# Optimization experiments

Measured on AMD Instinct MI355X. Metric: run time of the kernel, lower is better.

## Reference

```python
import jax, jax.numpy as jnp
import numpy as np

EPS = 1e-5  # rms_norm_eps

def rmsnorm(x, w, eps=EPS):
    xf = x.astype(jnp.float32)
    n = xf * jax.lax.rsqrt(jnp.mean(xf * xf, axis=-1, keepdims=True) + eps)
    return n.astype(x.dtype) * w

def setup_inputs() -> dict:
    key = jax.random.key(0)
    ks = jax.random.split(key, 8)
    B, S, E = 2, 2048, 2048
    H, M, D = 16, 2048, 128  # heads, memory slots, head_dim; H*D == E
    return {
        "query": jax.random.normal(ks[0], (B, S, E), jnp.float32),
        "storedpatterns": jax.random.normal(ks[1], (H, M, D), jnp.float32) * 0.02,
        "wq": jax.random.normal(ks[2], (H * D, E), jnp.float32) * (1.0 / np.sqrt(E)),
        "wk": jax.random.normal(ks[3], (D, D), jnp.float32) * (1.0 / np.sqrt(D)),
        "wv": jax.random.normal(ks[4], (D, D), jnp.float32) * (1.0 / np.sqrt(D)),
        "beta": jnp.ones((1, H, 1, 1), jnp.float32),
        "norm_q_w": jnp.ones((E,), jnp.float32),
        "norm_r_w": jnp.ones((H * D,), jnp.float32),
    }

def reference(query, storedpatterns, wq, wk, wv, beta, norm_q_w, norm_r_w):
    B, S, E = query.shape
    H, M, D = storedpatterns.shape
    # RMSNorm query, project to multi-head queries [B,H,S,D]
    qn = rmsnorm(query, norm_q_w)
    q = jnp.einsum('bse,fe->bsf', qn, wq).reshape(B, S, H, D).transpose(0, 2, 1, 3)
    # per-head K/V projections of stored memory patterns [H,M,D]
    k = jnp.einsum('hmd,ed->hme', storedpatterns, wk)
    v = jnp.einsum('hmd,ed->hme', storedpatterns, wv)
    # beta-scaled attention over memory slots
    scores = jnp.einsum('bhsd,hmd->bhsm', q, k) * beta / jnp.sqrt(jnp.float32(D))
    attn = jax.nn.softmax(scores, axis=-1)
    retrieved = jnp.einsum('bhsm,hmd->bhsd', attn, v)  # [B,H,S,D]
    retrieved = retrieved.transpose(0, 2, 1, 3).reshape(B, S, H * D)
    retrieved = rmsnorm(retrieved, norm_r_w)
    # combine_method='add' (pattern_dim == emb_dim, no dim projection)
    return query + retrieved
```

## Files before the change

kernel.cpp:

```cpp
#include <hip/hip_runtime.h>
#include <hip/hip_bf16.h>
#include <stdint.h>

typedef __attribute__((ext_vector_type(8))) short bf16x8;
typedef __attribute__((ext_vector_type(4))) float f32x4;
typedef __attribute__((ext_vector_type(8))) unsigned short u16x8;
typedef __attribute__((ext_vector_type(4))) unsigned short u16x4;
typedef __attribute__((ext_vector_type(2))) unsigned long long ull2;
typedef __attribute__((ext_vector_type(8))) int i32x8;

#define B_ 2
#define S_ 2048
#define E_ 2048
#define H_ 16
#define M_ 2048
#define D_ 128

#define MFMA16(a, b, c) __builtin_amdgcn_mfma_f32_16x16x32_bf16(a, b, c, 0, 0, 0)
#define MFMA8(a, b, c) __builtin_amdgcn_mfma_f32_16x16x32_fp8_fp8(a, b, c, 0, 0, 0)
#define MFMAS(a, b, c) __builtin_amdgcn_mfma_scale_f32_16x16x128_f8f6f4( \
    a, b, c, 0, 0, 0, 127, 0, 127)

union U32x8 { ull2 u2[2]; long long q[4]; i32x8 v; };

__device__ inline unsigned short f2bf(float f) {
  union { float f; unsigned u; } v; v.f = f;
  unsigned r = v.u + 0x7FFFu + ((v.u >> 16) & 1u);
  return (unsigned short)(r >> 16);
}
__device__ inline float bf2f(unsigned short h) {
  union { unsigned u; float f; } v; v.u = ((unsigned)h) << 16;
  return v.f;
}

__device__ inline unsigned char f2e8(float f) {
  return (unsigned char)(__builtin_amdgcn_cvt_pk_fp8_f32(f, f, 0, false) & 0xFF);
}
__device__ inline uint32_t pk4e8(float a, float b, float c, float d) {
  uint32_t w = 0;
  w = (uint32_t)__builtin_amdgcn_cvt_pk_fp8_f32(a, b, (int)w, false);
  w = (uint32_t)__builtin_amdgcn_cvt_pk_fp8_f32(c, d, (int)w, true);
  return w;
}

__device__ inline float exp2a(float x) {
  float r;
  asm("v_exp_f32 %0, %1" : "=v"(r) : "v"(x));
  return r;
}

__device__ inline void gload_lds16(const void* g, void* l) {
  __builtin_amdgcn_global_load_lds(
      (__attribute__((address_space(1))) void*)g,
      (__attribute__((address_space(3))) void*)l, 16, 0, 0);
}

__device__ inline bf16x8 pack8(float4 f0, float4 f1) {
  bf16x8 o;
  o[0] = (short)f2bf(f0.x); o[1] = (short)f2bf(f0.y);
  o[2] = (short)f2bf(f0.z); o[3] = (short)f2bf(f0.w);
  o[4] = (short)f2bf(f1.x); o[5] = (short)f2bf(f1.y);
  o[6] = (short)f2bf(f1.z); o[7] = (short)f2bf(f1.w);
  return o;
}

__device__ inline float block_sum(float v) {
  __shared__ float red[4];
  #pragma unroll
  for (int o = 32; o > 0; o >>= 1) v += __shfl_xor(v, o);
  int tid = threadIdx.x;
  if ((tid & 63) == 0) red[tid >> 6] = v;
  __syncthreads();
  return red[0] + red[1] + red[2] + red[3];
}

__device__ inline int pi_pos(int c) {
  return (c & ~127) | (((c >> 3) & 3) * 32) | (((c >> 5) & 3) * 8) | (c & 7);
}

#define PREP_PROJ 512
#define PREP_CONV 2048
#define PREP_NORM 4096
__global__ __launch_bounds__(256, 2) void prep_kernel(
    const float* __restrict__ query, const float* __restrict__ sp,
    const float* __restrict__ wq, const float* __restrict__ wk,
    const float* __restrict__ wv, const float* __restrict__ nqw,
    unsigned char* __restrict__ wqb, unsigned char* __restrict__ qn,
    unsigned char* __restrict__ kout, unsigned char* __restrict__ vtout)
{
  const int bid = blockIdx.x;
  const int tid = threadIdx.x;

  if (bid < PREP_PROJ) {
    const int idx = bid;
    const int m0 = (idx & 31) * 64;
    const int h = idx >> 5;
    const int wave = tid >> 6, lane = tid & 63;
    const int r = lane & 15, g = lane >> 4;
    const int wm = (wave >> 1) * 32, wn = (wave & 1) * 64;
    const float* spb = sp + ((size_t)h * M_ + m0) * D_;
    f32x4 acck[2][4] = {};
    f32x4 accv[2][4] = {};
    #pragma unroll
    for (int kc = 0; kc < 4; ++kc) {
      bf16x8 a[2], bk[4], bv[4];
      #pragma unroll
      for (int m = 0; m < 2; ++m) {
        const float* p = spb + (size_t)(wm + m * 16 + r) * D_ + kc * 32 + g * 8;
        a[m] = pack8(*(const float4*)p, *(const float4*)(p + 4));
      }
      #pragma unroll
      for (int n = 0; n < 4; ++n) {
        const float* pk = wk + (size_t)(wn + n * 16 + r) * D_ + kc * 32 + g * 8;
        bk[n] = pack8(*(const float4*)pk, *(const float4*)(pk + 4));
        const float* pv = wv + (size_t)(wn + n * 16 + r) * D_ + kc * 32 + g * 8;
        bv[n] = pack8(*(const float4*)pv, *(const float4*)(pv + 4));
      }
      #pragma unroll
      for (int m = 0; m < 2; ++m)
        #pragma unroll
        for (int n = 0; n < 4; ++n) {
          acck[m][n] = MFMA16(a[m], bk[n], acck[m][n]);
          accv[m][n] = MFMA16(a[m], bv[n], accv[m][n]);
        }
    }
    #pragma unroll
    for (int m = 0; m < 2; ++m)
      #pragma unroll
      for (int n = 0; n < 4; ++n)
        #pragma unroll
        for (int i = 0; i < 4; ++i) {
          int d = wn + n * 16 + r;
          kout[((size_t)h * M_ + m0 + wm + m * 16 + g * 4 + i) * D_ + pi_pos(d)]
              = f2e8(acck[m][n][i] * 32.0f);
          int mc = m0 + wm + m * 16 + g * 4 + i;
          int mp = (mc & ~127) | (pi_pos(mc & 127));
          vtout[((size_t)h * D_ + wn + n * 16 + r) * M_ + mp]
              = f2e8(accv[m][n][i] * 32.0f);
        }
  } else if (bid < PREP_PROJ + PREP_CONV) {
    int i = (bid - PREP_PROJ) * 256 + tid;
    const float* p = wq + (size_t)i * 8;
    float4 a = *(const float4*)p, b = *(const float4*)(p + 4);
    uint2 pk;
    pk.x = pk4e8(a.x, a.y, a.z, a.w);
    pk.y = pk4e8(b.x, b.y, b.z, b.w);
    size_t flat = (size_t)i * 8;
    int c = (int)(flat & (E_ - 1));
    *(uint2*)(wqb + (flat - c) + pi_pos(c)) = pk;
  } else {
    const int row = bid - (PREP_PROJ + PREP_CONV);
    const float* xr = query + (size_t)row * E_;
    float4 v0 = ((const float4*)xr)[tid * 2];
    float4 v1 = ((const float4*)xr)[tid * 2 + 1];
    float ss = v0.x*v0.x + v0.y*v0.y + v0.z*v0.z + v0.w*v0.w
             + v1.x*v1.x + v1.y*v1.y + v1.z*v1.z + v1.w*v1.w;
    float tot = block_sum(ss);
    float sc = rsqrtf(tot * (1.0f / E_) + 1e-5f);
    float vals[8] = {v0.x, v0.y, v0.z, v0.w, v1.x, v1.y, v1.z, v1.w};
    const float* wr = nqw + tid * 8;
    float f[8];
    #pragma unroll
    for (int j = 0; j < 8; ++j) f[j] = vals[j] * sc * wr[j];
    uint2 pk;
    pk.x = pk4e8(f[0], f[1], f[2], f[3]);
    pk.y = pk4e8(f[4], f[5], f[6], f[7]);
    *(uint2*)(qn + (size_t)row * E_ + pi_pos(tid * 8)) = pk;
  }
}

__global__ __launch_bounds__(256) void gemm_qproj(
    const unsigned char* __restrict__ A, const unsigned char* __restrict__ B,
    unsigned char* __restrict__ C, int M, int N, int K)
{
  __shared__ __align__(16) unsigned char As[128 * 128];
  __shared__ __align__(16) unsigned char Bs[128 * 128];
  const int nwg = gridDim.x;
  const int cpx = nwg >> 3;
  const int swz = (blockIdx.x & 7) * cpx + (blockIdx.x >> 3);
  const int mt = M >> 7;
  const int bm = (swz % mt) * 128;
  const int bn = (swz / mt) * 128;
  const int tid = threadIdx.x;
  const int wave = tid >> 6, lane = tid & 63;
  const int r = lane & 15, g = lane >> 4;
  const int wm = (wave >> 1) * 64, wn = (wave & 1) * 64;
  const int fx = (r & 7) << 4;

  f32x4 acc[4][4] = {};

  for (int k0 = 0; k0 < K; k0 += 128) {
    #pragma unroll
    for (int c = 0; c < 4; ++c) {
      int chunk = wave * 4 + c;
      int off = chunk * 1024 + lane * 16;
      int row = off >> 7;
      int cb = (off & 127) ^ ((row & 7) << 4);
      gload_lds16(A + (size_t)(bm + row) * K + k0 + cb, (char*)As + chunk * 1024);
      gload_lds16(B + (size_t)(bn + row) * K + k0 + cb, (char*)Bs + chunk * 1024);
    }
    __syncthreads();
    {
      U32x8 af[4], bf[4];
      #pragma unroll
      for (int m = 0; m < 4; ++m) {
        const char* pr = (const char*)As + (wm + m * 16 + r) * 128;
        af[m].u2[0] = *(const ull2*)(pr + ((g * 32) ^ fx));
        af[m].u2[1] = *(const ull2*)(pr + ((g * 32 + 16) ^ fx));
      }
      #pragma unroll
      for (int n = 0; n < 4; ++n) {
        const char* pr = (const char*)Bs + (wn + n * 16 + r) * 128;
        bf[n].u2[0] = *(const ull2*)(pr + ((g * 32) ^ fx));
        bf[n].u2[1] = *(const ull2*)(pr + ((g * 32 + 16) ^ fx));
      }
      #pragma unroll
      for (int m = 0; m < 4; ++m)
        #pragma unroll
        for (int n = 0; n < 4; ++n)
          acc[m][n] = MFMAS(af[m].v, bf[n].v, acc[m][n]);
    }
    __syncthreads();
  }
  #pragma unroll
  for (int m = 0; m < 4; ++m)
    #pragma unroll
    for (int n = 0; n < 4; ++n)
      #pragma unroll
      for (int i = 0; i < 4; ++i) {
        int row = bm + wm + m * 16 + g * 4 + i;
        int col = bn + wn + n * 16 + r;
        C[(size_t)row * N + col] = f2e8(acc[m][n][i]);
      }
}

__global__ __launch_bounds__(512, 4) void attn_kernel(
    const unsigned char* __restrict__ q,
    const unsigned char* __restrict__ kb,
    const unsigned char* __restrict__ vtb,
    const float* __restrict__ beta,
    unsigned short* __restrict__ ret)
{
  __shared__ __align__(16) unsigned char Ks[2][128 * 128];
  __shared__ __align__(16) unsigned char Vs[2][128 * 128];
  __shared__ __align__(16) unsigned char Ps[8][16 * 128];
  const int s0 = blockIdx.x * 128;
  const int h = blockIdx.y;
  const int b = blockIdx.z;
  const int tid = threadIdx.x, wave = tid >> 6, lane = tid & 63;
  const int r = lane & 15, g = lane >> 4;
  const int fx = (r & 7) << 4;
  const float escale = beta[h] * (0.08838834764831845f * 1.4426950408889634f / 32.0f);

  U32x8 qv;
  {
    const unsigned char* qr0 =
        q + ((size_t)(b * S_) + s0 + wave * 16 + r) * E_ + h * D_;
    #pragma unroll
    for (int kc = 0; kc < 4; ++kc)
      qv.q[kc] = *(const long long*)(qr0 + kc * 32 + g * 8);
  }

  const unsigned char* Kh = kb + (size_t)h * M_ * D_;
  const unsigned char* Vh = vtb + (size_t)h * D_ * M_;
  unsigned char* Pw = Ps[wave];
  U32x8 ones8;
  #pragma unroll
  for (int i = 0; i < 4; ++i) ones8.q[i] = 0x3838383838383838LL;

  f32x4 o[8] = {};
  f32x4 ol = {};

  auto stage = [&](int buf, int m0) {
    #pragma unroll
    for (int c = 0; c < 2; ++c) {
      int chunk = wave * 2 + c;
      int off = chunk * 1024 + lane * 16;
      int row = off >> 7;
      int cb = (off & 127) ^ ((row & 7) << 4);
      gload_lds16(Kh + (size_t)(m0 + row) * 128 + cb, (char*)Ks[buf] + chunk * 1024);
      gload_lds16(Vh + (size_t)row * M_ + m0 + cb, (char*)Vs[buf] + chunk * 1024);
    }
  };

  stage(0, 0);
  __syncthreads();

  int cur = 0;
  for (int t = 0; t < M_ / 128; ++t) {
    if (t + 1 < M_ / 128) stage(cur ^ 1, (t + 1) * 128);

    const unsigned char* Kc = Ks[cur];
    const unsigned char* Vc = Vs[cur];

    f32x4 s[8] = {};
    __builtin_amdgcn_s_setprio(1);
    #pragma unroll
    for (int nf = 0; nf < 8; ++nf) {
      const unsigned char* kr = Kc + (nf * 16 + r) * 128;
      U32x8 kf;
      kf.u2[0] = *(const ull2*)(kr + ((g * 32) ^ fx));
      kf.u2[1] = *(const ull2*)(kr + ((g * 32 + 16) ^ fx));
      s[nf] = MFMAS(kf.v, qv.v, s[nf]);
    }
    __builtin_amdgcn_s_setprio(0);

    #pragma unroll
    for (int nf = 0; nf < 8; ++nf) {
      float p0 = exp2a(s[nf][0] * escale), p1 = exp2a(s[nf][1] * escale),
            p2 = exp2a(s[nf][2] * escale), p3 = exp2a(s[nf][3] * escale);
      uint32_t w = 0;
      w = (uint32_t)__builtin_amdgcn_cvt_pk_fp8_f32(p0, p1, (int)w, false);
      w = (uint32_t)__builtin_amdgcn_cvt_pk_fp8_f32(p2, p3, (int)w, true);
      int pbase = ((nf & 1) * 2 + (g >> 1)) * 32 + (nf >> 1) * 8 + (g & 1) * 4;
      *(uint32_t*)(Pw + r * 128 + (pbase ^ fx)) = w;
    }

    U32x8 pv;
    pv.u2[0] = *(const ull2*)(Pw + r * 128 + ((g * 32) ^ fx));
    pv.u2[1] = *(const ull2*)(Pw + r * 128 + ((g * 32 + 16) ^ fx));
    __builtin_amdgcn_s_setprio(1);
    ol = MFMAS(pv.v, ones8.v, ol);
    #pragma unroll
    for (int nf2 = 0; nf2 < 8; ++nf2) {
      const unsigned char* vr = Vc + (nf2 * 16 + r) * 128;
      U32x8 vf;
      vf.u2[0] = *(const ull2*)(vr + ((g * 32) ^ fx));
      vf.u2[1] = *(const ull2*)(vr + ((g * 32 + 16) ^ fx));
      o[nf2] = MFMAS(pv.v, vf.v, o[nf2]);
    }
    __builtin_amdgcn_s_setprio(0);
    __syncthreads();
    cur ^= 1;
  }

  float invA[4];
  #pragma unroll
  for (int i = 0; i < 4; ++i) invA[i] = 0.03125f / ol[i];
  unsigned short* rr = ret + ((size_t)(b * S_) + s0 + wave * 16) * E_ + h * D_;
  #pragma unroll
  for (int nf2 = 0; nf2 < 8; ++nf2)
    #pragma unroll
    for (int i = 0; i < 4; ++i)
      rr[(size_t)(g * 4 + i) * E_ + nf2 * 16 + r] = f2bf(o[nf2][i] * invA[i]);
}

__global__ __launch_bounds__(256) void final_kernel(
    const unsigned short* __restrict__ ret, const float* __restrict__ w,
    const float* __restrict__ query, float* __restrict__ out)
{
  const int row = blockIdx.x;
  const int tid = threadIdx.x;
  u16x8 hv = *(const u16x8*)(ret + (size_t)row * E_ + tid * 8);
  float x[8];
  float ss = 0.f;
  #pragma unroll
  for (int j = 0; j < 8; ++j) { x[j] = bf2f(hv[j]); ss += x[j] * x[j]; }
  float tot = block_sum(ss);
  float sc = rsqrtf(tot * (1.0f / E_) + 1e-5f);
  const float* qr = query + (size_t)row * E_ + tid * 8;
  const float* wr = w + tid * 8;
  float o[8];
  #pragma unroll
  for (int j = 0; j < 8; ++j) o[j] = qr[j] + x[j] * sc * wr[j];
  float4* op = (float4*)(out + (size_t)row * E_ + tid * 8);
  op[0] = make_float4(o[0], o[1], o[2], o[3]);
  op[1] = make_float4(o[4], o[5], o[6], o[7]);
}

extern "C" void kernel_launch(void* const* d_in, const int* in_sizes, int n_in,
                              void* d_out, int out_size, void* d_ws, size_t ws_size,
                              hipStream_t stream) {
  const float* query = (const float*)d_in[0];
  const float* sp    = (const float*)d_in[1];
  const float* wq    = (const float*)d_in[2];
  const float* wk    = (const float*)d_in[3];
  const float* wv    = (const float*)d_in[4];
  const float* beta  = (const float*)d_in[5];
  const float* nqw   = (const float*)d_in[6];
  const float* nrw   = (const float*)d_in[7];
  float* out = (float*)d_out;

  char* ws = (char*)d_ws;
  unsigned char*  wqb = (unsigned char*)(ws + 0);
  unsigned char*  qn  = (unsigned char*)(ws + ((size_t)8 << 20));
  unsigned char*  qb  = (unsigned char*)(ws + ((size_t)24 << 20));
  unsigned char*  kb  = (unsigned char*)(ws + ((size_t)32 << 20));
  unsigned char*  vtb = (unsigned char*)(ws + ((size_t)36 << 20));
  unsigned short* ret = (unsigned short*)(ws + ((size_t)40 << 20));

  prep_kernel<<<PREP_PROJ + PREP_CONV + PREP_NORM, 256, 0, stream>>>(
      query, sp, wq, wk, wv, nqw, wqb, qn, kb, vtb);
  gemm_qproj<<<(B_ * S_ / 128) * (E_ / 128), 256, 0, stream>>>(
      qn, wqb, qb, B_ * S_, E_, E_);
  attn_kernel<<<dim3(S_ / 128, H_, B_), 512, 0, stream>>>(qb, kb, vtb, beta, ret);
  final_kernel<<<B_ * S_, 256, 0, stream>>>(ret, nrw, query, out);
}
```

Before: 122.9 us.

## Process two 16-row query tiles per wave in attention kernel with 4 waves

The attention block drops from 8 waves to 4, and each wave now handles two 16-row query tiles (rows r and r+64). Each K and V fragment read from LDS is then reused for two MFMAs, which halves LDS fragment traffic per MFMA. Each wave does more K/V staging loads per tile, and register pressure roughly doubles for the accumulators. That pressure could cut occupancy or cause spills, and there are fewer waves available to hide latency.

Measured after the change: 120.1 us. 1.02x faster.

```diff
diff --git a/kernel.cpp b/kernel.cpp
--- a/kernel.cpp
+++ b/kernel.cpp
@@ -234,7 +234,7 @@
       }
 }
 
-__global__ __launch_bounds__(512, 4) void attn_kernel(
+__global__ __launch_bounds__(256, 2) void attn_kernel(
     const unsigned char* __restrict__ q,
     const unsigned char* __restrict__ kb,
     const unsigned char* __restrict__ vtb,
@@ -243,7 +243,7 @@
 {
   __shared__ __align__(16) unsigned char Ks[2][128 * 128];
   __shared__ __align__(16) unsigned char Vs[2][128 * 128];
-  __shared__ __align__(16) unsigned char Ps[8][16 * 128];
+  __shared__ __align__(16) unsigned char Ps[4][32 * 128];
   const int s0 = blockIdx.x * 128;
   const int h = blockIdx.y;
   const int b = blockIdx.z;
@@ -252,13 +252,16 @@
   const int fx = (r & 7) << 4;
   const float escale = beta[h] * (0.08838834764831845f * 1.4426950408889634f / 32.0f);
 
-  U32x8 qv;
+  U32x8 qv0, qv1;
   {
     const unsigned char* qr0 =
         q + ((size_t)(b * S_) + s0 + wave * 16 + r) * E_ + h * D_;
-    #pragma unroll
-    for (int kc = 0; kc < 4; ++kc)
-      qv.q[kc] = *(const long long*)(qr0 + kc * 32 + g * 8);
+    const unsigned char* qr1 = qr0 + (size_t)64 * E_;
+    #pragma unroll
+    for (int kc = 0; kc < 4; ++kc) {
+      qv0.q[kc] = *(const long long*)(qr0 + kc * 32 + g * 8);
+      qv1.q[kc] = *(const long long*)(qr1 + kc * 32 + g * 8);
+    }
   }
 
   const unsigned char* Kh = kb + (size_t)h * M_ * D_;
@@ -268,13 +271,13 @@
   #pragma unroll
   for (int i = 0; i < 4; ++i) ones8.q[i] = 0x3838383838383838LL;
 
-  f32x4 o[8] = {};
-  f32x4 ol = {};
+  f32x4 o0[8] = {}, o1[8] = {};
+  f32x4 ol0 = {}, ol1 = {};
 
   auto stage = [&](int buf, int m0) {
     #pragma unroll
-    for (int c = 0; c < 2; ++c) {
-      int chunk = wave * 2 + c;
+    for (int c = 0; c < 4; ++c) {
+      int chunk = wave * 4 + c;
       int off = chunk * 1024 + lane * 16;
       int row = off >> 7;
       int cb = (off & 127) ^ ((row & 7) << 4);
@@ -293,7 +296,7 @@
     const unsigned char* Kc = Ks[cur];
     const unsigned char* Vc = Vs[cur];
 
-    f32x4 s[8] = {};
+    f32x4 sA[8] = {}, sB[8] = {};
     __builtin_amdgcn_s_setprio(1);
     #pragma unroll
     for (int nf = 0; nf < 8; ++nf) {
@@ -301,48 +304,70 @@
       U32x8 kf;
       kf.u2[0] = *(const ull2*)(kr + ((g * 32) ^ fx));
       kf.u2[1] = *(const ull2*)(kr + ((g * 32 + 16) ^ fx));
-      s[nf] = MFMAS(kf.v, qv.v, s[nf]);
+      sA[nf] = MFMAS(kf.v, qv0.v, sA[nf]);
+      sB[nf] = MFMAS(kf.v, qv1.v, sB[nf]);
     }
     __builtin_amdgcn_s_setprio(0);
 
     #pragma unroll
     for (int nf = 0; nf < 8; ++nf) {
-      float p0 = exp2a(s[nf][0] * escale), p1 = exp2a(s[nf][1] * escale),
-            p2 = exp2a(s[nf][2] * escale), p3 = exp2a(s[nf][3] * escale);
-      uint32_t w = 0;
-      w = (uint32_t)__builtin_amdgcn_cvt_pk_fp8_f32(p0, p1, (int)w, false);
-      w = (uint32_t)__builtin_amdgcn_cvt_pk_fp8_f32(p2, p3, (int)w, true);
       int pbase = ((nf & 1) * 2 + (g >> 1)) * 32 + (nf >> 1) * 8 + (g & 1) * 4;
-      *(uint32_t*)(Pw + r * 128 + (pbase ^ fx)) = w;
-    }
-
-    U32x8 pv;
-    pv.u2[0] = *(const ull2*)(Pw + r * 128 + ((g * 32) ^ fx));
-    pv.u2[1] = *(const ull2*)(Pw + r * 128 + ((g * 32 + 16) ^ fx));
+      {
+        float p0 = exp2a(sA[nf][0] * escale), p1 = exp2a(sA[nf][1] * escale),
+              p2 = exp2a(sA[nf][2] * escale), p3 = exp2a(sA[nf][3] * escale);
+        *(uint32_t*)(Pw + r * 128 + (pbase ^ fx)) = pk4e8(p0, p1, p2, p3);
+      }
+      {
+        float p0 = exp2a(sB[nf][0] * escale), p1 = exp2a(sB[nf][1] * escale),
+              p2 = exp2a(sB[nf][2] * escale), p3 = exp2a(sB[nf][3] * escale);
+        *(uint32_t*)(Pw + (16 + r) * 128 + (pbase ^ fx)) = pk4e8(p0, p1, p2, p3);
+      }
+    }
+
+    U32x8 pv0, pv1;
+    pv0.u2[0] = *(const ull2*)(Pw + r * 128 + ((g * 32) ^ fx));
+    pv0.u2[1] = *(const ull2*)(Pw + r * 128 + ((g * 32 + 16) ^ fx));
+    pv1.u2[0] = *(const ull2*)(Pw + (16 + r) * 128 + ((g * 32) ^ fx));
+    pv1.u2[1] = *(const ull2*)(Pw + (16 + r) * 128 + ((g * 32 + 16) ^ fx));
     __builtin_amdgcn_s_setprio(1);
-    ol = MFMAS(pv.v, ones8.v, ol);
+    ol0 = MFMAS(pv0.v, ones8.v, ol0);
+    ol1 = MFMAS(pv1.v, ones8.v, ol1);
     #pragma unroll
     for (int nf2 = 0; nf2 < 8; ++nf2) {
       const unsigned char* vr = Vc + (nf2 * 16 + r) * 128;
       U32x8 vf;
       vf.u2[0] = *(const ull2*)(vr + ((g * 32) ^ fx));
       vf.u2[1] = *(const ull2*)(vr + ((g * 32 + 16) ^ fx));
-      o[nf2] = MFMAS(pv.v, vf.v, o[nf2]);
+      o0[nf2] = MFMAS(pv0.v, vf.v, o0[nf2]);
+      o1[nf2] = MFMAS(pv1.v, vf.v, o1[nf2]);
     }
     __builtin_amdgcn_s_setprio(0);
     __syncthreads();
     cur ^= 1;
   }
 
-  float invA[4];
-  #pragma unroll
-  for (int i = 0; i < 4; ++i) invA[i] = 0.03125f / ol[i];
-  unsigned short* rr = ret + ((size_t)(b * S_) + s0 + wave * 16) * E_ + h * D_;
-  #pragma unroll
-  for (int nf2 = 0; nf2 < 8; ++nf2)
-    #pragma unroll
-    for (int i = 0; i < 4; ++i)
-      rr[(size_t)(g * 4 + i) * E_ + nf2 * 16 + r] = f2bf(o[nf2][i] * invA[i]);
+  {
+    float inv[4];
+    #pragma unroll
+    for (int i = 0; i < 4; ++i) inv[i] = 0.03125f / ol0[i];
+    unsigned short* rr = ret + ((size_t)(b * S_) + s0 + wave * 16) * E_ + h * D_;
+    #pragma unroll
+    for (int nf2 = 0; nf2 < 8; ++nf2)
+      #pragma unroll
+      for (int i = 0; i < 4; ++i)
+        rr[(size_t)(g * 4 + i) * E_ + nf2 * 16 + r] = f2bf(o0[nf2][i] * inv[i]);
+  }
+  {
+    float inv[4];
+    #pragma unroll
+    for (int i = 0; i < 4; ++i) inv[i] = 0.03125f / ol1[i];
+    unsigned short* rr = ret + ((size_t)(b * S_) + s0 + 64 + wave * 16) * E_ + h * D_;
+    #pragma unroll
+    for (int nf2 = 0; nf2 < 8; ++nf2)
+      #pragma unroll
+      for (int i = 0; i < 4; ++i)
+        rr[(size_t)(g * 4 + i) * E_ + nf2 * 16 + r] = f2bf(o1[nf2][i] * inv[i]);
+  }
 }
 
 __global__ __launch_bounds__(256) void final_kernel(
@@ -393,6 +418,6 @@
       query, sp, wq, wk, wv, nqw, wqb, qn, kb, vtb);
   gemm_qproj<<<(B_ * S_ / 128) * (E_ / 128), 256, 0, stream>>>(
       qn, wqb, qb, B_ * S_, E_, E_);
-  attn_kernel<<<dim3(S_ / 128, H_, B_), 512, 0, stream>>>(qb, kb, vtb, beta, ret);
+  attn_kernel<<<dim3(S_ / 128, H_, B_), 256, 0, stream>>>(qb, kb, vtb, beta, ret);
   final_kernel<<<B_ * S_, 256, 0, stream>>>(ret, nrw, query, out);
 }
```
